# Optimization experiments

Measured on AMD Instinct MI355X. Metric: run time of the kernel, lower is better.

The kernel has to match this reference:

```python
import jax, jax.numpy as jnp
import numpy as np

B, L, D, H = 4, 2048, 1024, 16
HD = D // H
EPS = 1e-5


def _layernorm(x, g, b):
    mu = jnp.mean(x, axis=-1, keepdims=True)
    var = jnp.mean(jnp.square(x - mu), axis=-1, keepdims=True)
    return (x - mu) * jax.lax.rsqrt(var + EPS) * g + b


def _rotate_half(x):
    x1, x2 = jnp.split(x, 2, axis=-1)
    return jnp.concatenate([-x2, x1], axis=-1)


def setup_inputs() -> dict:
    key = jax.random.key(0)
    ks = jax.random.split(key, 12)
    s = 0.02
    return {
        "x": jax.random.normal(ks[0], (B, L, D), jnp.float32),
        "pos_cos": jax.random.uniform(ks[1], (B, L, D), jnp.float32),
        "pos_sin": jax.random.uniform(ks[2], (B, L, D), jnp.float32),
        "attn_mask": jnp.zeros((B, L), jnp.float32),
        "Wq": jax.random.normal(ks[3], (D, D), jnp.float32) * s,
        "Wk": jax.random.normal(ks[4], (D, D), jnp.float32) * s,
        "Wv": jax.random.normal(ks[5], (D, D), jnp.float32) * s,
        "Wo": jax.random.normal(ks[6], (D, D), jnp.float32) * s,
        "W1": jax.random.normal(ks[7], (D, 2 * D), jnp.float32) * s,
        "W2": jax.random.normal(ks[8], (D, D), jnp.float32) * s,
        "g1": jnp.ones((D,), jnp.float32),
        "b1": jnp.zeros((D,), jnp.float32),
        "g2": jnp.ones((D,), jnp.float32),
        "b2": jnp.zeros((D,), jnp.float32),
    }


def reference(x, pos_cos, pos_sin, attn_mask, Wq, Wk, Wv, Wo, W1, W2, g1, b1, g2, b2):
    # --- attention sublayer (pre-LN) ---
    residual = x
    xn = _layernorm(x, g1, b1)
    split_heads = lambda t: t.reshape(B, L, H, HD).transpose(0, 2, 1, 3)  # [B,H,L,hd]
    q = split_heads(xn @ Wq)
    k = split_heads(xn @ Wk)
    v = split_heads(xn @ Wv)
    cos = split_heads(pos_cos)
    sin = split_heads(pos_sin)
    q = q * cos + _rotate_half(q) * sin
    k = k * cos + _rotate_half(k) * sin
    scores = jnp.einsum('bhqd,bhkd->bhqk', q, k) / np.float32(np.sqrt(HD))
    scores = scores + attn_mask[:, None, None, :]  # additive mask over keys
    probs = jax.nn.softmax(scores, axis=-1)
    ctx = jnp.einsum('bhqk,bhkd->bhqd', probs, v)
    ctx = ctx.transpose(0, 2, 1, 3).reshape(B, L, D)
    x = residual + ctx @ Wo
    # --- SwiGLU FFN sublayer (pre-LN) ---
    residual = x
    xn = _layernorm(x, g2, b2)
    h = xn @ W1
    x1, x2 = h[..., :D], h[..., D:]
    ffn = (jax.nn.silu(x1) * x2) @ W2
    return residual + ffn
```

## Files before the change

kernel.cpp:

```cpp
#include <hip/hip_runtime.h>
#include <hip/hip_bf16.h>

typedef unsigned short ushort_t;
typedef short short8 __attribute__((ext_vector_type(8)));
typedef unsigned short u16x4 __attribute__((ext_vector_type(4)));
typedef float f32x4 __attribute__((ext_vector_type(4)));
typedef int int2v __attribute__((ext_vector_type(2)));
typedef int int4v __attribute__((ext_vector_type(4)));

#define MFMA_BF16 __builtin_amdgcn_mfma_f32_16x16x32_bf16

#define GLDS16(g, l) __builtin_amdgcn_global_load_lds( \
    (__attribute__((address_space(1))) void*)(g), \
    (__attribute__((address_space(3))) void*)(l), 16, 0, 0)

__device__ __forceinline__ unsigned short f2bf(float f) {
  union { float f; unsigned u; } v; v.f = f;
  unsigned r = v.u + 0x7FFFu + ((v.u >> 16) & 1u);
  return (unsigned short)(r >> 16);
}
__device__ __forceinline__ float bf2f(unsigned short h) {
  union { unsigned u; float f; } v; v.u = ((unsigned)h) << 16;
  return v.f;
}
__device__ __forceinline__ unsigned pack_bf2(float a, float b) {
  __hip_bfloat162 t = __float22bfloat162_rn(float2{a, b});
  union { __hip_bfloat162 h; unsigned u; } v; v.h = t;
  return v.u;
}
__device__ __forceinline__ float exp2_raw(float x) {
  float r;
  asm volatile("v_exp_f32 %0, %1" : "=v"(r) : "v"(x));
  return r;
}

#define BB 4
#define LL 2048
#define DD 1024
#define HH 16
#define HD 64
#define NROW (BB * LL)
#define LOG2E 1.4426950408889634f

template <int PERM>
__global__ __launch_bounds__(256) void wconv(const float* __restrict__ W,
                                             ushort_t* __restrict__ WT,
                                             int R, int C) {
  __shared__ float tile[32][33];
  const int ct = blockIdx.x * 32, rt = blockIdx.y * 32;
  const int tx = threadIdx.x & 31, ty = threadIdx.x >> 5;
#pragma unroll
  for (int j = 0; j < 4; ++j)
    tile[ty + j * 8][tx] = W[(size_t)(rt + ty + j * 8) * C + ct + tx];
  __syncthreads();
  int orow0 = ct;
  if (PERM)
    orow0 = (ct < 1024) ? ((ct >> 5) * 64) : ((((ct - 1024) >> 5) * 64) + 32);
#pragma unroll
  for (int j = 0; j < 4; ++j)
    WT[(size_t)(orow0 + ty + j * 8) * R + rt + tx] = f2bf(tile[tx][ty + j * 8]);
}

template <int BIN>
__global__ __launch_bounds__(256) void ln_kernel(const void* __restrict__ xin,
                                                 const float* __restrict__ g,
                                                 const float* __restrict__ bt,
                                                 ushort_t* __restrict__ out) {
  const int row = blockIdx.x, t = threadIdx.x;
  f32x4 v;
  if (BIN) {
    const u16x4 hv =
        *(const u16x4*)((const ushort_t*)xin + (size_t)row * DD + t * 4);
    v[0] = bf2f(hv[0]); v[1] = bf2f(hv[1]);
    v[2] = bf2f(hv[2]); v[3] = bf2f(hv[3]);
  } else {
    v = *(const f32x4*)((const float*)xin + (size_t)row * DD + t * 4);
  }
  float s = v[0] + v[1] + v[2] + v[3];
  float sq = v[0] * v[0] + v[1] * v[1] + v[2] * v[2] + v[3] * v[3];
#pragma unroll
  for (int off = 1; off < 64; off <<= 1) {
    s += __shfl_xor(s, off);
    sq += __shfl_xor(sq, off);
  }
  __shared__ float aw[4], aq[4];
  if ((t & 63) == 0) { aw[t >> 6] = s; aq[t >> 6] = sq; }
  __syncthreads();
  s = aw[0] + aw[1] + aw[2] + aw[3];
  sq = aq[0] + aq[1] + aq[2] + aq[3];
  const float mu = s * (1.f / DD);
  const float var = sq * (1.f / DD) - mu * mu;
  const float rs = rsqrtf(var + 1e-5f);
  u16x4 o;
#pragma unroll
  for (int j = 0; j < 4; ++j) {
    const int c = t * 4 + j;
    o[j] = f2bf((v[j] - mu) * rs * g[c] + bt[c]);
  }
  *(u16x4*)(out + (size_t)row * DD + t * 4) = o;
}

template <int EPI>
__global__ __launch_bounds__(256) void gemm_bt(const ushort_t* __restrict__ A,
                                               const ushort_t* __restrict__ BT,
                                               ushort_t* __restrict__ Cb,
                                               float* __restrict__ Cf,
                                               const float* __restrict__ residf,
                                               const ushort_t* __restrict__ residb,
                                               int M, int N, int K) {
  __shared__ ushort_t As[128 * 32];
  __shared__ ushort_t Bs[128 * 32];
  const int tid = threadIdx.x;
  const int lane = tid & 63;
  const int w = tid >> 6;
  const int wr = w >> 1, wc = w & 1;
  const int nwg = gridDim.x * gridDim.y;
  const int orig = blockIdx.y * gridDim.x + blockIdx.x;
  const int wg = (orig & 7) * (nwg >> 3) + (orig >> 3);
  const int bm = (wg / gridDim.x) * 128, bn = (wg % gridDim.x) * 128;
  const int lrow = lane >> 2;
  const int lcol = (lane & 3) * 8;
  const int fr = lane & 15;
  const int fo = (lane >> 4) * 8;
  f32x4 acc[4][4];
#pragma unroll
  for (int m = 0; m < 4; ++m)
#pragma unroll
    for (int n = 0; n < 4; ++n) acc[m][n] = (f32x4){0.f, 0.f, 0.f, 0.f};

  const int nk = K >> 5;
  for (int kt = 0; kt < nk; ++kt) {
    __syncthreads();
#pragma unroll
    for (int c = 0; c < 2; ++c) {
      const int seg = c * 4 + w;
      const int row = seg * 16 + lrow;
      GLDS16(A + (size_t)(bm + row) * K + kt * 32 + lcol, &As[seg * 512]);
      GLDS16(BT + (size_t)(bn + row) * K + kt * 32 + lcol, &Bs[seg * 512]);
    }
    asm volatile("s_waitcnt vmcnt(0)" ::: "memory");
    __syncthreads();
    short8 af[4], bf_[4];
#pragma unroll
    for (int m = 0; m < 4; ++m)
      af[m] = *(const short8*)&As[(wr * 64 + m * 16 + fr) * 32 + fo];
#pragma unroll
    for (int n = 0; n < 4; ++n)
      bf_[n] = *(const short8*)&Bs[(wc * 64 + n * 16 + fr) * 32 + fo];
#pragma unroll
    for (int m = 0; m < 4; ++m)
#pragma unroll
      for (int n = 0; n < 4; ++n)
        acc[m][n] = MFMA_BF16(af[m], bf_[n], acc[m][n], 0, 0, 0);
  }
  const int r0 = (lane >> 4) * 4;
#pragma unroll
  for (int m = 0; m < 4; ++m)
#pragma unroll
    for (int n = 0; n < 4; ++n)
#pragma unroll
      for (int r = 0; r < 4; ++r) {
        const int gr = bm + wr * 64 + m * 16 + r0 + r;
        const int gc = bn + wc * 64 + n * 16 + fr;
        const size_t o = (size_t)gr * N + gc;
        if (EPI == 1) Cb[o] = f2bf(residf[o] + acc[m][n][r]);
        else          Cf[o] = bf2f(residb[o]) + acc[m][n][r];
      }
}

template <int EPI>
__global__ __launch_bounds__(256) void gemm_f(
    const ushort_t* __restrict__ A, const ushort_t* __restrict__ BT,
    const float* __restrict__ pcos, const float* __restrict__ psin,
    ushort_t* __restrict__ qh, ushort_t* __restrict__ kh,
    ushort_t* __restrict__ vt, ushort_t* __restrict__ gact,
    int M, int N, int K) {
  __shared__ ushort_t As[128 * 32];
  __shared__ ushort_t Bs[128 * 32];
  const int tid = threadIdx.x;
  const int lane = tid & 63;
  const int w = tid >> 6;
  const int wr = w >> 1, wc = w & 1;
  const int nwg = gridDim.x * gridDim.y;
  const int orig = blockIdx.y * gridDim.x + blockIdx.x;
  const int wg = (orig & 7) * (nwg >> 3) + (orig >> 3);
  const int bm = (wg / gridDim.x) * 128, bn = (wg % gridDim.x) * 128;
  const int lrow = lane >> 2;
  const int lcol = (lane & 3) * 8;
  const int fr = lane & 15;
  const int hi = lane >> 4;
  const int fo = hi * 8;
  f32x4 acc[4][4];
#pragma unroll
  for (int m = 0; m < 4; ++m)
#pragma unroll
    for (int n = 0; n < 4; ++n) acc[m][n] = (f32x4){0.f, 0.f, 0.f, 0.f};

  const int nk = K >> 5;
  for (int kt = 0; kt < nk; ++kt) {
    __syncthreads();
#pragma unroll
    for (int c = 0; c < 2; ++c) {
      const int seg = c * 4 + w;
      const int row = seg * 16 + lrow;
      GLDS16(A + (size_t)(bm + row) * K + kt * 32 + lcol, &As[seg * 512]);
      GLDS16(BT + (size_t)(bn + row) * K + kt * 32 + lcol, &Bs[seg * 512]);
    }
    asm volatile("s_waitcnt vmcnt(0)" ::: "memory");
    __syncthreads();
    short8 af[4], bf_[4];
#pragma unroll
    for (int m = 0; m < 4; ++m)
      af[m] = *(const short8*)&As[(wr * 64 + m * 16 + fr) * 32 + fo];
#pragma unroll
    for (int n = 0; n < 4; ++n)
      bf_[n] = *(const short8*)&Bs[(wc * 64 + n * 16 + fr) * 32 + fo];
#pragma unroll
    for (int m = 0; m < 4; ++m)
#pragma unroll
      for (int n = 0; n < 4; ++n)
        acc[m][n] = MFMA_BF16(af[m], bf_[n], acc[m][n], 0, 0, 0);
  }

  if (EPI == 1) {
    const int gcol = bn + wc * 64;
    const int region = gcol >> 10;
    const int h = (gcol & 1023) >> 6;
    const int b = bm >> 11;
    if (region < 2) {
      const float qs = (region == 0) ? 0.125f : 1.0f;
      ushort_t* dstbuf = (region == 0) ? qh : kh;
      const int dbase = h * 64;
#pragma unroll
      for (int m = 0; m < 4; ++m) {
        const int gr0 = bm + wr * 64 + m * 16 + hi * 4;
#pragma unroll
        for (int r = 0; r < 4; ++r) {
          const int gr = gr0 + r;
          const int l = gr & 2047;
          const float* pcr = pcos + (size_t)gr * DD + dbase;
          const float* psr = psin + (size_t)gr * DD + dbase;
          ushort_t* dst = dstbuf + ((size_t)(b * HH + h) * LL + l) * HD;
#pragma unroll
          for (int n = 0; n < 2; ++n) {
            const int dlo = n * 16 + fr;
            const float xlo = acc[m][n][r], xhi = acc[m][n + 2][r];
            dst[dlo] = f2bf((xlo * pcr[dlo] - xhi * psr[dlo]) * qs);
            dst[dlo + 32] = f2bf((xhi * pcr[dlo + 32] + xlo * psr[dlo + 32]) * qs);
          }
        }
      }
    } else {
      const size_t bhv = (size_t)(b * HH + h);
      const int l0 = (bm & 2047) + wr * 64;
      const int lt = l0 >> 6;
#pragma unroll
      for (int m = 0; m < 4; ++m) {
        const int slotb = 32 * (m >> 1) + 8 * hi + 4 * (m & 1);
#pragma unroll
        for (int n = 0; n < 4; ++n) {
          const int hd = n * 16 + fr;
          u16x4 wv;
          wv[0] = f2bf(acc[m][n][0]);
          wv[1] = f2bf(acc[m][n][1]);
          wv[2] = f2bf(acc[m][n][2]);
          wv[3] = f2bf(acc[m][n][3]);
          *(u16x4*)(vt + (bhv * HD + hd) * LL + lt * 64 + slotb) = wv;
        }
      }
    }
  } else {
    const int jbase = ((bn + wc * 64) >> 6) * 32;
#pragma unroll
    for (int m = 0; m < 4; ++m) {
      const int gr0 = bm + wr * 64 + m * 16 + hi * 4;
#pragma unroll
      for (int r = 0; r < 4; ++r) {
        ushort_t* dst = gact + (size_t)(gr0 + r) * DD + jbase;
#pragma unroll
        for (int n = 0; n < 2; ++n) {
          const float x1 = acc[m][n][r];
          const float x2 = acc[m][n + 2][r];
          dst[n * 16 + fr] = f2bf(x1 / (1.f + __expf(-x1)) * x2);
        }
      }
    }
  }
}

__global__ __launch_bounds__(512) void attn_kernel(
    const ushort_t* __restrict__ qh, const ushort_t* __restrict__ kh,
    const ushort_t* __restrict__ vt, const float* __restrict__ mask,
    ushort_t* __restrict__ ctx) {
  const int tid = threadIdx.x, lane = tid & 63, w = tid >> 6;
  const int bh = blockIdx.y, b = bh >> 4, h = bh & 15;
  const int q0 = blockIdx.x * 128;
  __shared__ ushort_t Ks[2][64 * 64];
  __shared__ ushort_t Vs[2][64 * 64];
  const int fr = lane & 15;
  const int hi = lane >> 4;
  const int fo = hi * 8;
  const int qrow = q0 + w * 16 + fr;
  const size_t qoff = ((size_t)bh * LL + qrow) * HD + fo;
  const short8 qf0 = *(const short8*)(qh + qoff);
  const short8 qf1 = *(const short8*)(qh + qoff + 32);
  short8 ones;
#pragma unroll
  for (int i = 0; i < 8; ++i) ones[i] = (short)0x3F80;

  f32x4 oacc[4];
  f32x4 lacc = (f32x4){0.f, 0.f, 0.f, 0.f};
#pragma unroll
  for (int m = 0; m < 4; ++m) oacc[m] = (f32x4){0.f, 0.f, 0.f, 0.f};

  const int lrow = lane >> 3;
  const int lcs = ((lane & 7) ^ lrow) * 8;
  const int rr = w * 8 + lrow;

  const float* mrow = mask + (size_t)b * LL;

  const int NT = LL / 128;
  for (int kt = 0; kt < NT; ++kt) {
    __syncthreads();
    GLDS16(kh + ((size_t)bh * LL + kt * 128 + rr) * HD + lcs, &Ks[0][w * 512]);
    GLDS16(kh + ((size_t)bh * LL + kt * 128 + 64 + rr) * HD + lcs,
           &Ks[1][w * 512]);
    GLDS16(vt + ((size_t)bh * HD + rr) * LL + kt * 128 + lcs, &Vs[0][w * 512]);
    GLDS16(vt + ((size_t)bh * HD + rr) * LL + kt * 128 + 64 + lcs,
           &Vs[1][w * 512]);
    f32x4 mk[8];
#pragma unroll
    for (int n = 0; n < 8; ++n)
      mk[n] = *(const f32x4*)(mrow + kt * 128 + n * 16 + hi * 4);
    asm volatile("s_waitcnt vmcnt(0)" ::: "memory");
    __syncthreads();

#pragma unroll
    for (int sub = 0; sub < 2; ++sub) {
      f32x4 s[4];
#pragma unroll
      for (int n = 0; n < 4; ++n) s[n] = mk[sub * 4 + n];
      __builtin_amdgcn_s_setprio(1);
#pragma unroll
      for (int n = 0; n < 4; ++n) {
        const int krow = n * 16 + fr;
#pragma unroll
        for (int c = 0; c < 2; ++c) {
          const int col = (c * 32 + fo) ^ ((fr & 7) * 8);
          const short8 kf = *(const short8*)&Ks[sub][krow * 64 + col];
          s[n] = MFMA_BF16(kf, c ? qf1 : qf0, s[n], 0, 0, 0);
        }
      }
      __builtin_amdgcn_s_setprio(0);
      unsigned pk[4][2];
#pragma unroll
      for (int n = 0; n < 4; ++n) {
        const float p0 = exp2_raw(s[n][0] * LOG2E);
        const float p1 = exp2_raw(s[n][1] * LOG2E);
        const float p2 = exp2_raw(s[n][2] * LOG2E);
        const float p3 = exp2_raw(s[n][3] * LOG2E);
        pk[n][0] = pack_bf2(p0, p1);
        pk[n][1] = pack_bf2(p2, p3);
      }
      __builtin_amdgcn_s_setprio(1);
#pragma unroll
      for (int c = 0; c < 2; ++c) {
        int4v pw = {(int)pk[2 * c][0], (int)pk[2 * c][1],
                    (int)pk[2 * c + 1][0], (int)pk[2 * c + 1][1]};
        union { int4v i; short8 s; } pf; pf.i = pw;
#pragma unroll
        for (int m = 0; m < 4; ++m) {
          const int row = m * 16 + fr;
          const int col = (c * 32 + fo) ^ ((fr & 7) * 8);
          const short8 vf = *(const short8*)&Vs[sub][row * 64 + col];
          oacc[m] = MFMA_BF16(vf, pf.s, oacc[m], 0, 0, 0);
        }
        lacc = MFMA_BF16(ones, pf.s, lacc, 0, 0, 0);
      }
      __builtin_amdgcn_s_setprio(0);
    }
  }
  const float inv = 1.f / lacc[0];
  const int q = q0 + w * 16 + fr;
  ushort_t* dst = ctx + ((size_t)b * LL + q) * DD + h * 64 + hi * 4;
#pragma unroll
  for (int m = 0; m < 4; ++m) {
    int2v val;
    val[0] = (int)pack_bf2(oacc[m][0] * inv, oacc[m][1] * inv);
    val[1] = (int)pack_bf2(oacc[m][2] * inv, oacc[m][3] * inv);
    *(int2v*)(dst + m * 16) = val;
  }
}

extern "C" void kernel_launch(void* const* d_in, const int* in_sizes, int n_in,
                              void* d_out, int out_size, void* d_ws,
                              size_t ws_size, hipStream_t stream) {
  const float* x = (const float*)d_in[0];
  const float* pcos = (const float*)d_in[1];
  const float* psin = (const float*)d_in[2];
  const float* mask = (const float*)d_in[3];
  const float* Wq = (const float*)d_in[4];
  const float* Wk = (const float*)d_in[5];
  const float* Wv = (const float*)d_in[6];
  const float* Wo = (const float*)d_in[7];
  const float* W1 = (const float*)d_in[8];
  const float* W2 = (const float*)d_in[9];
  const float* g1 = (const float*)d_in[10];
  const float* b1 = (const float*)d_in[11];
  const float* g2 = (const float*)d_in[12];
  const float* b2 = (const float*)d_in[13];
  float* out = (float*)d_out;
  char* ws = (char*)d_ws;

  ushort_t* WQKVT = (ushort_t*)(ws);
  ushort_t* WOT = (ushort_t*)(ws + 6291456);
  ushort_t* W1T = (ushort_t*)(ws + 8388608);
  ushort_t* W2T = (ushort_t*)(ws + 12582912);
  ushort_t* XN = (ushort_t*)(ws + 14680064);
  ushort_t* GACT = (ushort_t*)(ws + 31457280 + 33554432);
  ushort_t* QH = (ushort_t*)(ws + 81788928);
  ushort_t* KH = (ushort_t*)(ws + 98566144);
  ushort_t* VT = (ushort_t*)(ws + 115343360);
  ushort_t* CTX = (ushort_t*)(ws + 132120576);
  ushort_t* XMIDB = (ushort_t*)(ws + 148897792);

  wconv<0><<<dim3(32, 32), 256, 0, stream>>>(Wq, WQKVT, 1024, 1024);
  wconv<0><<<dim3(32, 32), 256, 0, stream>>>(Wk, WQKVT + 1024 * 1024, 1024, 1024);
  wconv<0><<<dim3(32, 32), 256, 0, stream>>>(Wv, WQKVT + 2 * 1024 * 1024, 1024, 1024);
  wconv<0><<<dim3(32, 32), 256, 0, stream>>>(Wo, WOT, 1024, 1024);
  wconv<1><<<dim3(64, 32), 256, 0, stream>>>(W1, W1T, 1024, 2048);
  wconv<0><<<dim3(32, 32), 256, 0, stream>>>(W2, W2T, 1024, 1024);

  ln_kernel<0><<<NROW, 256, 0, stream>>>(x, g1, b1, XN);
  gemm_f<1><<<dim3(24, 64), 256, 0, stream>>>(XN, WQKVT, pcos, psin, QH, KH,
                                              VT, nullptr, NROW, 3072, 1024);
  attn_kernel<<<dim3(16, 64), 512, 0, stream>>>(QH, KH, VT, mask, CTX);
  gemm_bt<1><<<dim3(8, 64), 256, 0, stream>>>(CTX, WOT, XMIDB, nullptr, x,
                                              nullptr, NROW, 1024, 1024);
  ln_kernel<1><<<NROW, 256, 0, stream>>>(XMIDB, g2, b2, XN);
  gemm_f<2><<<dim3(16, 64), 256, 0, stream>>>(XN, W1T, nullptr, nullptr,
                                              nullptr, nullptr, nullptr, GACT,
                                              NROW, 2048, 1024);
  gemm_bt<2><<<dim3(8, 64), 256, 0, stream>>>(GACT, W2T, nullptr, out, nullptr,
                                              XMIDB, NROW, 1024, 1024);
}
```

Measured before the change: 372.6 us.

## Use 256x256 tiles with 4-stage LDS pipeline and swizzle for fused GEMMs

Replaces the fused QKV and W1 GEMMs with a 512-thread kernel that computes 256x256 output tiles. It prefetches K-slices three stages ahead into a 4-buffer LDS ring through direct global-to-LDS loads, and XOR-swizzles LDS columns to avoid bank conflicts. It also raises wave priority around the MFMA block. The goal is to hide global load latency and increase data reuse per tile. In exchange it uses 128 KB of LDS per block and far more accumulator registers, which may limit occupancy and leave a small grid of 384 and 256 blocks.

```diff
diff --git a/kernel.cpp b/kernel.cpp
--- a/kernel.cpp
+++ b/kernel.cpp
@@ -13,6 +13,8 @@
 #define GLDS16(g, l) __builtin_amdgcn_global_load_lds( \
     (__attribute__((address_space(1))) void*)(g), \
     (__attribute__((address_space(3))) void*)(l), 16, 0, 0)
+
+#define WAITVM(n) asm volatile("s_waitcnt vmcnt(" #n ")" ::: "memory")
 
 __device__ __forceinline__ unsigned short f2bf(float f) {
   union { float f; unsigned u; } v; v.f = f;
@@ -169,61 +171,77 @@
 }
 
 template <int EPI>
-__global__ __launch_bounds__(256) void gemm_f(
+__global__ __launch_bounds__(512, 2) void gemm9(
     const ushort_t* __restrict__ A, const ushort_t* __restrict__ BT,
     const float* __restrict__ pcos, const float* __restrict__ psin,
     ushort_t* __restrict__ qh, ushort_t* __restrict__ kh,
     ushort_t* __restrict__ vt, ushort_t* __restrict__ gact,
     int M, int N, int K) {
-  __shared__ ushort_t As[128 * 32];
-  __shared__ ushort_t Bs[128 * 32];
-  const int tid = threadIdx.x;
-  const int lane = tid & 63;
-  const int w = tid >> 6;
-  const int wr = w >> 1, wc = w & 1;
+  __shared__ ushort_t SA[4][256 * 32];
+  __shared__ ushort_t SB[4][256 * 32];
+  const int tid = threadIdx.x, lane = tid & 63, w = tid >> 6;
+  const int wm = w >> 2, wn = w & 3;
   const int nwg = gridDim.x * gridDim.y;
   const int orig = blockIdx.y * gridDim.x + blockIdx.x;
   const int wg = (orig & 7) * (nwg >> 3) + (orig >> 3);
-  const int bm = (wg / gridDim.x) * 128, bn = (wg % gridDim.x) * 128;
-  const int lrow = lane >> 2;
-  const int lcol = (lane & 3) * 8;
-  const int fr = lane & 15;
-  const int hi = lane >> 4;
-  const int fo = hi * 8;
-  f32x4 acc[4][4];
-#pragma unroll
-  for (int m = 0; m < 4; ++m)
+  const int bm = (wg / gridDim.x) * 256, bn = (wg % gridDim.x) * 256;
+  const int fr = lane & 15, hi = lane >> 4;
+  const int NS = K >> 5;
+  const int srow = lane >> 2;
+  const int sc = ((lane & 3) ^ ((lane >> 3) & 3)) * 8;
+  const int rdo = (hi ^ ((fr >> 1) & 3)) * 8;
+
+  f32x4 acc[8][4];
+#pragma unroll
+  for (int m = 0; m < 8; ++m)
 #pragma unroll
     for (int n = 0; n < 4; ++n) acc[m][n] = (f32x4){0.f, 0.f, 0.f, 0.f};
 
-  const int nk = K >> 5;
-  for (int kt = 0; kt < nk; ++kt) {
-    __syncthreads();
-#pragma unroll
-    for (int c = 0; c < 2; ++c) {
-      const int seg = c * 4 + w;
-      const int row = seg * 16 + lrow;
-      GLDS16(A + (size_t)(bm + row) * K + kt * 32 + lcol, &As[seg * 512]);
-      GLDS16(BT + (size_t)(bn + row) * K + kt * 32 + lcol, &Bs[seg * 512]);
+#define STG9(X, base, kt, SX)                                                \
+  {                                                                          \
+    _Pragma("unroll") for (int l = 0; l < 2; ++l) {                          \
+      const int seg = l * 8 + w;                                             \
+      GLDS16(X + (size_t)((base) + seg * 16 + srow) * K + (kt) * 32 + sc,    \
+             &SX[(kt) & 3][seg * 512]);                                      \
+    }                                                                        \
+  }
+
+  STG9(A, bm, 0, SA); STG9(BT, bn, 0, SB);
+  STG9(A, bm, 1, SA); STG9(BT, bn, 1, SB);
+  STG9(A, bm, 2, SA); STG9(BT, bn, 2, SB);
+  WAITVM(8);
+
+#pragma unroll 1
+  for (int s = 0; s < NS; ++s) {
+    asm volatile("" ::: "memory");
+    __builtin_amdgcn_s_barrier();
+    if (s + 3 < NS) {
+      STG9(A, bm, s + 3, SA); STG9(BT, bn, s + 3, SB);
+      WAITVM(8);
+    } else if (s + 2 < NS) {
+      WAITVM(4);
+    } else {
+      WAITVM(0);
     }
-    asm volatile("s_waitcnt vmcnt(0)" ::: "memory");
-    __syncthreads();
-    short8 af[4], bf_[4];
-#pragma unroll
-    for (int m = 0; m < 4; ++m)
-      af[m] = *(const short8*)&As[(wr * 64 + m * 16 + fr) * 32 + fo];
+    const int buf = s & 3;
+    short8 af[8], bfr[4];
+#pragma unroll
+    for (int m = 0; m < 8; ++m)
+      af[m] = *(const short8*)&SA[buf][(wm * 128 + m * 16 + fr) * 32 + rdo];
 #pragma unroll
     for (int n = 0; n < 4; ++n)
-      bf_[n] = *(const short8*)&Bs[(wc * 64 + n * 16 + fr) * 32 + fo];
-#pragma unroll
-    for (int m = 0; m < 4; ++m)
+      bfr[n] = *(const short8*)&SB[buf][(wn * 64 + n * 16 + fr) * 32 + rdo];
+    __builtin_amdgcn_s_setprio(1);
+#pragma unroll
+    for (int m = 0; m < 8; ++m)
 #pragma unroll
       for (int n = 0; n < 4; ++n)
-        acc[m][n] = MFMA_BF16(af[m], bf_[n], acc[m][n], 0, 0, 0);
+        acc[m][n] = MFMA_BF16(af[m], bfr[n], acc[m][n], 0, 0, 0);
+    __builtin_amdgcn_s_setprio(0);
   }
 
   if (EPI == 1) {
-    const int gcol = bn + wc * 64;
+    const int gcol = bn + wn * 64;
     const int region = gcol >> 10;
     const int h = (gcol & 1023) >> 6;
     const int b = bm >> 11;
@@ -232,8 +250,8 @@
       ushort_t* dstbuf = (region == 0) ? qh : kh;
       const int dbase = h * 64;
 #pragma unroll
-      for (int m = 0; m < 4; ++m) {
-        const int gr0 = bm + wr * 64 + m * 16 + hi * 4;
+      for (int m = 0; m < 8; ++m) {
+        const int gr0 = bm + wm * 128 + m * 16 + hi * 4;
 #pragma unroll
         for (int r = 0; r < 4; ++r) {
           const int gr = gr0 + r;
@@ -252,11 +270,11 @@
       }
     } else {
       const size_t bhv = (size_t)(b * HH + h);
-      const int l0 = (bm & 2047) + wr * 64;
-      const int lt = l0 >> 6;
-#pragma unroll
-      for (int m = 0; m < 4; ++m) {
-        const int slotb = 32 * (m >> 1) + 8 * hi + 4 * (m & 1);
+#pragma unroll
+      for (int m = 0; m < 8; ++m) {
+        const int l0 = (bm & 2047) + wm * 128 + m * 16;
+        const int lt = l0 >> 6;
+        const int slotb = 32 * ((m >> 1) & 1) + 8 * hi + 4 * (m & 1);
 #pragma unroll
         for (int n = 0; n < 4; ++n) {
           const int hd = n * 16 + fr;
@@ -270,10 +288,10 @@
       }
     }
   } else {
-    const int jbase = ((bn + wc * 64) >> 6) * 32;
-#pragma unroll
-    for (int m = 0; m < 4; ++m) {
-      const int gr0 = bm + wr * 64 + m * 16 + hi * 4;
+    const int jbase = ((bn + wn * 64) >> 6) * 32;
+#pragma unroll
+    for (int m = 0; m < 8; ++m) {
+      const int gr0 = bm + wm * 128 + m * 16 + hi * 4;
 #pragma unroll
       for (int r = 0; r < 4; ++r) {
         ushort_t* dst = gact + (size_t)(gr0 + r) * DD + jbase;
@@ -286,6 +304,7 @@
       }
     }
   }
+#undef STG9
 }
 
 __global__ __launch_bounds__(512) void attn_kernel(
@@ -432,15 +451,15 @@
   wconv<0><<<dim3(32, 32), 256, 0, stream>>>(W2, W2T, 1024, 1024);
 
   ln_kernel<0><<<NROW, 256, 0, stream>>>(x, g1, b1, XN);
-  gemm_f<1><<<dim3(24, 64), 256, 0, stream>>>(XN, WQKVT, pcos, psin, QH, KH,
-                                              VT, nullptr, NROW, 3072, 1024);
+  gemm9<1><<<dim3(12, 32), 512, 0, stream>>>(XN, WQKVT, pcos, psin, QH, KH, VT,
+                                             nullptr, NROW, 3072, 1024);
   attn_kernel<<<dim3(16, 64), 512, 0, stream>>>(QH, KH, VT, mask, CTX);
   gemm_bt<1><<<dim3(8, 64), 256, 0, stream>>>(CTX, WOT, XMIDB, nullptr, x,
                                               nullptr, NROW, 1024, 1024);
   ln_kernel<1><<<NROW, 256, 0, stream>>>(XMIDB, g2, b2, XN);
-  gemm_f<2><<<dim3(16, 64), 256, 0, stream>>>(XN, W1T, nullptr, nullptr,
-                                              nullptr, nullptr, nullptr, GACT,
-                                              NROW, 2048, 1024);
+  gemm9<2><<<dim3(8, 32), 512, 0, stream>>>(XN, W1T, nullptr, nullptr, nullptr,
+                                            nullptr, nullptr, GACT, NROW, 2048,
+                                            1024);
   gemm_bt<2><<<dim3(8, 64), 256, 0, stream>>>(GACT, W2T, nullptr, out, nullptr,
                                               XMIDB, NROW, 1024, 1024);
 }
```

Measured after the change: 361.7 us. 2.9% less time.

## Double GEMM K-tile to 64 with XOR-swizzled LDS layout, unify GEMM kernels

Applied to the files above, without the earlier changes.

Merges the two GEMM templates into one kernel with four epilogue modes and doubles the K step per iteration from 32 to 64. LDS tiles are stored with an XOR swizzle on 16-byte chunks to avoid bank conflicts in the fragment reads. This halves the number of barrier/wait rounds per GEMM and feeds 32 MFMAs per sync instead of 16. In exchange it doubles LDS use per block, which may reduce occupancy, and the loads are still not overlapped with compute.

```diff
diff --git a/kernel.cpp b/kernel.cpp
--- a/kernel.cpp
+++ b/kernel.cpp
@@ -101,15 +101,16 @@
 }
 
 template <int EPI>
-__global__ __launch_bounds__(256) void gemm_bt(const ushort_t* __restrict__ A,
-                                               const ushort_t* __restrict__ BT,
-                                               ushort_t* __restrict__ Cb,
-                                               float* __restrict__ Cf,
-                                               const float* __restrict__ residf,
-                                               const ushort_t* __restrict__ residb,
-                                               int M, int N, int K) {
-  __shared__ ushort_t As[128 * 32];
-  __shared__ ushort_t Bs[128 * 32];
+__global__ __launch_bounds__(256) void gemm64(
+    const ushort_t* __restrict__ A, const ushort_t* __restrict__ BT,
+    const float* __restrict__ pcos, const float* __restrict__ psin,
+    ushort_t* __restrict__ qh, ushort_t* __restrict__ kh,
+    ushort_t* __restrict__ vt, ushort_t* __restrict__ gact,
+    ushort_t* __restrict__ Cb, float* __restrict__ Cf,
+    const float* __restrict__ residf, const ushort_t* __restrict__ residb,
+    int M, int N, int K) {
+  __shared__ ushort_t As[128 * 64];
+  __shared__ ushort_t Bs[128 * 64];
   const int tid = threadIdx.x;
   const int lane = tid & 63;
   const int w = tid >> 6;
@@ -118,108 +119,49 @@
   const int orig = blockIdx.y * gridDim.x + blockIdx.x;
   const int wg = (orig & 7) * (nwg >> 3) + (orig >> 3);
   const int bm = (wg / gridDim.x) * 128, bn = (wg % gridDim.x) * 128;
-  const int lrow = lane >> 2;
-  const int lcol = (lane & 3) * 8;
   const int fr = lane & 15;
-  const int fo = (lane >> 4) * 8;
+  const int hi = lane >> 4;
+  const int srow8 = lane >> 3;
+  const int schunk = (lane & 7) ^ srow8;
   f32x4 acc[4][4];
 #pragma unroll
   for (int m = 0; m < 4; ++m)
 #pragma unroll
     for (int n = 0; n < 4; ++n) acc[m][n] = (f32x4){0.f, 0.f, 0.f, 0.f};
 
-  const int nk = K >> 5;
+  const int nk = K >> 6;
   for (int kt = 0; kt < nk; ++kt) {
     __syncthreads();
 #pragma unroll
-    for (int c = 0; c < 2; ++c) {
-      const int seg = c * 4 + w;
-      const int row = seg * 16 + lrow;
-      GLDS16(A + (size_t)(bm + row) * K + kt * 32 + lcol, &As[seg * 512]);
-      GLDS16(BT + (size_t)(bn + row) * K + kt * 32 + lcol, &Bs[seg * 512]);
+    for (int c = 0; c < 4; ++c) {
+      const int rbase = w * 32 + c * 8;
+      const int grow = rbase + srow8;
+      GLDS16(A + (size_t)(bm + grow) * K + kt * 64 + schunk * 8,
+             &As[rbase * 64]);
+      GLDS16(BT + (size_t)(bn + grow) * K + kt * 64 + schunk * 8,
+             &Bs[rbase * 64]);
     }
     asm volatile("s_waitcnt vmcnt(0)" ::: "memory");
     __syncthreads();
-    short8 af[4], bf_[4];
-#pragma unroll
-    for (int m = 0; m < 4; ++m)
-      af[m] = *(const short8*)&As[(wr * 64 + m * 16 + fr) * 32 + fo];
-#pragma unroll
-    for (int n = 0; n < 4; ++n)
-      bf_[n] = *(const short8*)&Bs[(wc * 64 + n * 16 + fr) * 32 + fo];
-#pragma unroll
-    for (int m = 0; m < 4; ++m)
-#pragma unroll
-      for (int n = 0; n < 4; ++n)
-        acc[m][n] = MFMA_BF16(af[m], bf_[n], acc[m][n], 0, 0, 0);
-  }
-  const int r0 = (lane >> 4) * 4;
-#pragma unroll
-  for (int m = 0; m < 4; ++m)
-#pragma unroll
-    for (int n = 0; n < 4; ++n)
-#pragma unroll
-      for (int r = 0; r < 4; ++r) {
-        const int gr = bm + wr * 64 + m * 16 + r0 + r;
-        const int gc = bn + wc * 64 + n * 16 + fr;
-        const size_t o = (size_t)gr * N + gc;
-        if (EPI == 1) Cb[o] = f2bf(residf[o] + acc[m][n][r]);
-        else          Cf[o] = bf2f(residb[o]) + acc[m][n][r];
-      }
-}
-
-template <int EPI>
-__global__ __launch_bounds__(256) void gemm_f(
-    const ushort_t* __restrict__ A, const ushort_t* __restrict__ BT,
-    const float* __restrict__ pcos, const float* __restrict__ psin,
-    ushort_t* __restrict__ qh, ushort_t* __restrict__ kh,
-    ushort_t* __restrict__ vt, ushort_t* __restrict__ gact,
-    int M, int N, int K) {
-  __shared__ ushort_t As[128 * 32];
-  __shared__ ushort_t Bs[128 * 32];
-  const int tid = threadIdx.x;
-  const int lane = tid & 63;
-  const int w = tid >> 6;
-  const int wr = w >> 1, wc = w & 1;
-  const int nwg = gridDim.x * gridDim.y;
-  const int orig = blockIdx.y * gridDim.x + blockIdx.x;
-  const int wg = (orig & 7) * (nwg >> 3) + (orig >> 3);
-  const int bm = (wg / gridDim.x) * 128, bn = (wg % gridDim.x) * 128;
-  const int lrow = lane >> 2;
-  const int lcol = (lane & 3) * 8;
-  const int fr = lane & 15;
-  const int hi = lane >> 4;
-  const int fo = hi * 8;
-  f32x4 acc[4][4];
-#pragma unroll
-  for (int m = 0; m < 4; ++m)
-#pragma unroll
-    for (int n = 0; n < 4; ++n) acc[m][n] = (f32x4){0.f, 0.f, 0.f, 0.f};
-
-  const int nk = K >> 5;
-  for (int kt = 0; kt < nk; ++kt) {
-    __syncthreads();
-#pragma unroll
-    for (int c = 0; c < 2; ++c) {
-      const int seg = c * 4 + w;
-      const int row = seg * 16 + lrow;
-      GLDS16(A + (size_t)(bm + row) * K + kt * 32 + lcol, &As[seg * 512]);
-      GLDS16(BT + (size_t)(bn + row) * K + kt * 32 + lcol, &Bs[seg * 512]);
+#pragma unroll
+    for (int khf = 0; khf < 2; ++khf) {
+      short8 af[4], bf_[4];
+#pragma unroll
+      for (int m = 0; m < 4; ++m) {
+        const int r = wr * 64 + m * 16 + fr;
+        af[m] = *(const short8*)&As[r * 64 + (((khf << 2) + hi) ^ (fr & 7)) * 8];
+      }
+#pragma unroll
+      for (int n = 0; n < 4; ++n) {
+        const int r = wc * 64 + n * 16 + fr;
+        bf_[n] = *(const short8*)&Bs[r * 64 + (((khf << 2) + hi) ^ (fr & 7)) * 8];
+      }
+#pragma unroll
+      for (int m = 0; m < 4; ++m)
+#pragma unroll
+        for (int n = 0; n < 4; ++n)
+          acc[m][n] = MFMA_BF16(af[m], bf_[n], acc[m][n], 0, 0, 0);
     }
-    asm volatile("s_waitcnt vmcnt(0)" ::: "memory");
-    __syncthreads();
-    short8 af[4], bf_[4];
-#pragma unroll
-    for (int m = 0; m < 4; ++m)
-      af[m] = *(const short8*)&As[(wr * 64 + m * 16 + fr) * 32 + fo];
-#pragma unroll
-    for (int n = 0; n < 4; ++n)
-      bf_[n] = *(const short8*)&Bs[(wc * 64 + n * 16 + fr) * 32 + fo];
-#pragma unroll
-    for (int m = 0; m < 4; ++m)
-#pragma unroll
-      for (int n = 0; n < 4; ++n)
-        acc[m][n] = MFMA_BF16(af[m], bf_[n], acc[m][n], 0, 0, 0);
   }
 
   if (EPI == 1) {
@@ -269,7 +211,7 @@
         }
       }
     }
-  } else {
+  } else if (EPI == 2) {
     const int jbase = ((bn + wc * 64) >> 6) * 32;
 #pragma unroll
     for (int m = 0; m < 4; ++m) {
@@ -285,6 +227,19 @@
         }
       }
     }
+  } else {
+#pragma unroll
+    for (int m = 0; m < 4; ++m)
+#pragma unroll
+      for (int n = 0; n < 4; ++n)
+#pragma unroll
+        for (int r = 0; r < 4; ++r) {
+          const int gr = bm + wr * 64 + m * 16 + hi * 4 + r;
+          const int gc = bn + wc * 64 + n * 16 + fr;
+          const size_t o = (size_t)gr * N + gc;
+          if (EPI == 3) Cb[o] = f2bf(residf[o] + acc[m][n][r]);
+          else          Cf[o] = bf2f(residb[o]) + acc[m][n][r];
+        }
   }
 }
 
@@ -432,15 +387,18 @@
   wconv<0><<<dim3(32, 32), 256, 0, stream>>>(W2, W2T, 1024, 1024);
 
   ln_kernel<0><<<NROW, 256, 0, stream>>>(x, g1, b1, XN);
-  gemm_f<1><<<dim3(24, 64), 256, 0, stream>>>(XN, WQKVT, pcos, psin, QH, KH,
-                                              VT, nullptr, NROW, 3072, 1024);
+  gemm64<1><<<dim3(24, 64), 256, 0, stream>>>(
+      XN, WQKVT, pcos, psin, QH, KH, VT, nullptr, nullptr, nullptr, nullptr,
+      nullptr, NROW, 3072, 1024);
   attn_kernel<<<dim3(16, 64), 512, 0, stream>>>(QH, KH, VT, mask, CTX);
-  gemm_bt<1><<<dim3(8, 64), 256, 0, stream>>>(CTX, WOT, XMIDB, nullptr, x,
-                                              nullptr, NROW, 1024, 1024);
+  gemm64<3><<<dim3(8, 64), 256, 0, stream>>>(
+      CTX, WOT, nullptr, nullptr, nullptr, nullptr, nullptr, nullptr, XMIDB,
+      nullptr, x, nullptr, NROW, 1024, 1024);
   ln_kernel<1><<<NROW, 256, 0, stream>>>(XMIDB, g2, b2, XN);
-  gemm_f<2><<<dim3(16, 64), 256, 0, stream>>>(XN, W1T, nullptr, nullptr,
-                                              nullptr, nullptr, nullptr, GACT,
-                                              NROW, 2048, 1024);
-  gemm_bt<2><<<dim3(8, 64), 256, 0, stream>>>(GACT, W2T, nullptr, out, nullptr,
-                                              XMIDB, NROW, 1024, 1024);
-}
+  gemm64<2><<<dim3(16, 64), 256, 0, stream>>>(
+      XN, W1T, nullptr, nullptr, nullptr, nullptr, nullptr, GACT, nullptr,
+      nullptr, nullptr, nullptr, NROW, 2048, 1024);
+  gemm64<4><<<dim3(8, 64), 256, 0, stream>>>(
+      GACT, W2T, nullptr, nullptr, nullptr, nullptr, nullptr, nullptr, nullptr,
+      out, nullptr, XMIDB, NROW, 1024, 1024);
+}
```

Result: faster. 337.1 us (-9.5%).
